# Optimization experiments

Hardware: AMD Instinct MI355X
Metric: run time of the kernel (lower is better)

## Reference

```python
import jax, jax.numpy as jnp
import numpy as np
from jax import lax

B, C, H, W = 16, 384, 28, 28
HEADS = 8


def _ln(x, g, b):
    mu = jnp.mean(x, axis=-1, keepdims=True)
    var = jnp.var(x, axis=-1, keepdims=True)
    return (x - mu) * lax.rsqrt(var + 1e-5) * g + b


def setup_inputs() -> dict:
    key = jax.random.key(0)
    ks = jax.random.split(key, 8)
    s = 0.02
    return {
        "cls_token": jax.random.normal(ks[0], (B, 1, C), dtype=jnp.float32),
        "x": jax.random.normal(ks[1], (B, C, H, W), dtype=jnp.float32),
        "conv_w": jax.random.normal(ks[2], (C, 1, 3, 3), dtype=jnp.float32) * s,
        "conv_b": jnp.zeros((C,), jnp.float32),
        "ln1_g": jnp.ones((C,), jnp.float32),
        "ln1_b": jnp.zeros((C,), jnp.float32),
        "qkv_w": jax.random.normal(ks[3], (3 * C, C), dtype=jnp.float32) * s,
        "proj_w": jax.random.normal(ks[4], (C, C), dtype=jnp.float32) * s,
        "proj_b": jnp.zeros((C,), jnp.float32),
        "ln2_g": jnp.ones((C,), jnp.float32),
        "ln2_b": jnp.zeros((C,), jnp.float32),
        "fc1_w": jax.random.normal(ks[5], (4 * C, C), dtype=jnp.float32) * s,
        "fc1_b": jnp.zeros((4 * C,), jnp.float32),
        "fc2_w": jax.random.normal(ks[6], (C, 4 * C), dtype=jnp.float32) * s,
        "fc2_b": jnp.zeros((C,), jnp.float32),
    }


def reference(cls_token, x, conv_w, conv_b, ln1_g, ln1_b, qkv_w, proj_w, proj_b,
              ln2_g, ln2_b, fc1_w, fc1_b, fc2_w, fc2_b):
    Bv, Cv, Hv, Wv = x.shape
    h = HEADS
    d = Cv // h
    # depthwise 3x3 positional conv (groups=dim), residual add
    pe = lax.conv_general_dilated(
        x, conv_w, window_strides=(1, 1), padding="SAME",
        feature_group_count=Cv,
        dimension_numbers=("NCHW", "OIHW", "NCHW")) + conv_b[None, :, None, None]
    x = x + pe
    x_patch = x.reshape(Bv, Cv, Hv * Wv).transpose(0, 2, 1)  # [B, HW, C]
    xc = jnp.concatenate([cls_token, x_patch], axis=1)       # [B, N, C]
    N = xc.shape[1]

    # --- Attention with inline global_attn stats (first-call / int sentinel path) ---
    y = _ln(xc, ln1_g, ln1_b)
    qkv = (y @ qkv_w.T).reshape(Bv, N, 3, h, d)
    q = qkv[:, :, 0].transpose(0, 2, 1, 3)  # [B, h, N, d]
    k = qkv[:, :, 1].transpose(0, 2, 1, 3)
    v = qkv[:, :, 2].transpose(0, 2, 1, 3)
    scale = d ** -0.5
    attn = jax.nn.softmax(jnp.einsum("bhnd,bhmd->bhnm", q, k) * scale, axis=-1)
    # per-token global attention statistic: mean over heads of cls row (excl. cls)
    global_attn = jnp.mean(attn[:, :, 0, 1:], axis=1)  # [B, N-1]
    o = jnp.einsum("bhnm,bhmd->bhnd", attn, v).transpose(0, 2, 1, 3).reshape(Bv, N, Cv)
    xc = xc + (o @ proj_w.T + proj_b)

    # --- MLP (GELU exact, matching torch nn.GELU default) ---
    y2 = _ln(xc, ln2_g, ln2_b)
    m = jax.nn.gelu(y2 @ fc1_w.T + fc1_b, approximate=False) @ fc2_w.T + fc2_b
    xc = xc + m

    cls_out = xc[:, :1]                                            # [B, 1, C]
    x_out = xc[:, 1:].transpose(0, 2, 1).reshape(Bv, Cv, Hv, Wv)    # [B, C, H, W]
    return cls_out, x_out, global_attn
```

## Files before the change

### kernel.cpp

```cpp
#include <hip/hip_runtime.h>
#include <hip/hip_bf16.h>

#define DI __device__ __forceinline__

typedef __attribute__((ext_vector_type(4))) float f32x4;
typedef __attribute__((ext_vector_type(8))) short bf16x8;
typedef __attribute__((ext_vector_type(4))) short bf16x4;

static constexpr int CB = 16;
static constexpr int CC = 384;
static constexpr int CH = 28, CW = 28;
static constexpr int CD = 48;
static constexpr int CN = 785;
static constexpr int CM = CB * CN;
static constexpr int C3 = 3 * CC;
static constexpr int CF = 4 * CC;
static constexpr int HW = CH * CW;
static constexpr int NP = 832;

DI short f2b(float f) {
  __hip_bfloat16 h = __float2bfloat16(f);
  return *reinterpret_cast<short*>(&h);
}
DI float b2f(short s) {
  union { unsigned u; float f; } x;
  x.u = ((unsigned)(unsigned short)s) << 16;
  return x.f;
}

DI void gload16(const short* g, short* l) {
  __builtin_amdgcn_global_load_lds((const __attribute__((address_space(1))) void*)g,
                                   (__attribute__((address_space(3))) void*)l, 16, 0, 0);
}

__global__ void k_misc(const float* __restrict__ cls, float* __restrict__ xc,
                       float* __restrict__ ga) {
  const int gid = blockIdx.x * 256 + threadIdx.x;
  if (gid < CB * HW) ga[gid] = 0.f;
  if (gid < CB * CC) {
    const int b = gid / CC, c = gid % CC;
    xc[((size_t)b * CN) * CC + c] = cls[gid];
  }
}

__global__ void k_wconv(const float* __restrict__ s0, const float* __restrict__ s1,
                        const float* __restrict__ s2, const float* __restrict__ s3,
                        short* __restrict__ dst) {
  const int gid = (blockIdx.x * 256 + threadIdx.x) * 4;
  if (gid >= 1769472) return;
  const float* s; int off;
  if (gid < 442368)       { s = s0; off = gid; }
  else if (gid < 589824)  { s = s1; off = gid - 442368; }
  else if (gid < 1179648) { s = s2; off = gid - 589824; }
  else                    { s = s3; off = gid - 1179648; }
  f32x4 v = *(const f32x4*)(s + off);
  bf16x4 o;
#pragma unroll
  for (int i = 0; i < 4; i++) o[i] = f2b(v[i]);
  *(bf16x4*)(dst + gid) = o;
}

__global__ __launch_bounds__(256) void k_conv_t(const float* __restrict__ x,
                                                const float* __restrict__ cw,
                                                const float* __restrict__ cb,
                                                float* __restrict__ xc) {
  __shared__ float T[64][65];
  __shared__ float Wc[64 * 9];
  __shared__ float Cbs[64];
  const int b = blockIdx.z;
  const int cc = blockIdx.y * 64;
  const int hw0 = blockIdx.x * 64;
  const int t = threadIdx.x;
  const int hwi = t & 63, ci0 = t >> 6;
  const int hw = hw0 + hwi;
  const int yy = hw / CW, xx = hw % CW;
  const int ci2 = t & 63, hb2 = t >> 6;

  for (int i = t; i < 64 * 9; i += 256) Wc[i] = cw[cc * 9 + i];
  if (t < 64) Cbs[t] = cb[cc + t];
  __syncthreads();
  if (hw < HW) {
#pragma unroll
    for (int j = 0; j < 16; j++) {
      const int cl = ci0 * 16 + j;
      const float* xp = x + ((size_t)(b * CC + cc + cl)) * HW;
      float acc = Cbs[cl];
      const float center = xp[yy * CW + xx];
#pragma unroll
      for (int ky = 0; ky < 3; ky++) {
        const int iy = yy + ky - 1;
        if (iy < 0 || iy >= CH) continue;
#pragma unroll
        for (int kx = 0; kx < 3; kx++) {
          const int ix = xx + kx - 1;
          if (ix < 0 || ix >= CW) continue;
          acc += Wc[cl * 9 + ky * 3 + kx] * xp[iy * CW + ix];
        }
      }
      T[cl][hwi] = center + acc;
    }
  }
  __syncthreads();
#pragma unroll
  for (int j = 0; j < 16; j++) {
    const int hwl = hb2 + j * 4;
    if (hw0 + hwl < HW)
      xc[((size_t)b * CN + 1 + hw0 + hwl) * CC + cc + ci2] = T[ci2][hwl];
  }
}

__global__ __launch_bounds__(256) void k_ln(const float* __restrict__ xin,
                                            const float* __restrict__ g,
                                            const float* __restrict__ bta,
                                            short* __restrict__ y, int Mtot) {
  const int row = blockIdx.x * 4 + (threadIdx.x >> 6);
  const int l = threadIdx.x & 63;
  if (row >= Mtot) return;
  const float* xr = xin + (size_t)row * CC;
  float v[6], s = 0.f, ss = 0.f;
#pragma unroll
  for (int i = 0; i < 6; i++) {
    v[i] = xr[l + i * 64];
    s += v[i];
    ss += v[i] * v[i];
  }
#pragma unroll
  for (int m = 1; m < 64; m <<= 1) { s += __shfl_xor(s, m); ss += __shfl_xor(ss, m); }
  const float mu = s * (1.f / CC);
  const float var = ss * (1.f / CC) - mu * mu;
  const float r = rsqrtf(var + 1e-5f);
#pragma unroll
  for (int i = 0; i < 6; i++) {
    const int c = l + i * 64;
    y[(size_t)row * CC + c] = f2b((v[i] - mu) * r * g[c] + bta[c]);
  }
}

template <int DOGELU, int DORES, int DOBIAS, int OUTBF>
__global__ __launch_bounds__(256) void k_gemm(const short* __restrict__ A,
                                              const short* __restrict__ W,
                                              const float* __restrict__ bias,
                                              const float* __restrict__ resid,
                                              void* __restrict__ out_,
                                              int M, int N, int K) {
  __shared__ short As[128 * 32];
  __shared__ short Bs[128 * 32];
  const int bm = blockIdx.x * 128, bn = blockIdx.y * 128;
  const int t = threadIdx.x, w = t >> 6, l = t & 63, g = l >> 4, li = l & 15;
  const int wm = (w >> 1) * 64, wn = (w & 1) * 64;

  const int srow = l >> 2;
  const int scol = (l & 3) * 8;
  const short* aSrc[2]; const short* bSrc[2];
  short* aDst[2]; short* bDst[2];
#pragma unroll
  for (int j = 0; j < 2; j++) {
    int arow = bm + w * 32 + j * 16 + srow; if (arow > M - 1) arow = M - 1;
    aSrc[j] = A + (size_t)arow * K + scol;
    aDst[j] = &As[(w * 32 + j * 16) * 32];
    const int brow = bn + w * 32 + j * 16 + srow;
    bSrc[j] = W + (size_t)brow * K + scol;
    bDst[j] = &Bs[(w * 32 + j * 16) * 32];
  }

  f32x4 acc[4][4] = {};
  const int nkt = K / 32;
  for (int kt = 0; kt < nkt; kt++) {
#pragma unroll
    for (int j = 0; j < 2; j++) {
      gload16(aSrc[j], aDst[j]);
      gload16(bSrc[j], bDst[j]);
      aSrc[j] += 32; bSrc[j] += 32;
    }
    __syncthreads();
    bf16x8 af[4], bf[4];
#pragma unroll
    for (int mi = 0; mi < 4; mi++)
      af[mi] = *(const bf16x8*)&As[(wm + mi * 16 + li) * 32 + g * 8];
#pragma unroll
    for (int ni = 0; ni < 4; ni++)
      bf[ni] = *(const bf16x8*)&Bs[(wn + ni * 16 + li) * 32 + g * 8];
#pragma unroll
    for (int mi = 0; mi < 4; mi++)
#pragma unroll
      for (int ni = 0; ni < 4; ni++)
        acc[mi][ni] = __builtin_amdgcn_mfma_f32_16x16x32_bf16(af[mi], bf[ni], acc[mi][ni], 0, 0, 0);
    __syncthreads();
  }

#pragma unroll
  for (int mi = 0; mi < 4; mi++)
#pragma unroll
    for (int ni = 0; ni < 4; ni++) {
      const int col = bn + wn + ni * 16 + li;
      float bv = 0.f;
      if constexpr (DOBIAS) bv = bias[col];
#pragma unroll
      for (int r = 0; r < 4; r++) {
        const int row = bm + wm + mi * 16 + g * 4 + r;
        if (row < M) {
          float v = acc[mi][ni][r] + bv;
          if constexpr (DOGELU) v = 0.5f * v * (1.f + erff(v * 0.7071067811865475f));
          if constexpr (DORES) v += resid[(size_t)row * N + col];
          if constexpr (OUTBF)
            ((short*)out_)[(size_t)row * N + col] = f2b(v);
          else
            ((float*)out_)[(size_t)row * N + col] = v;
        }
      }
    }
}

__global__ __launch_bounds__(256) void k_vt(const short* __restrict__ qkv,
                                            short* __restrict__ vt) {
  __shared__ short Tl[48 * 71];
  const int n0 = blockIdx.x * 64;
  const int bh = blockIdx.y;
  const int b = bh >> 3, h = bh & 7;
  const int t = threadIdx.x;
  const size_t bbase = (size_t)b * CN;
#pragma unroll
  for (int it = 0; it < 2; it++) {
    const int gi = t + it * 256;
    if (gi < 384) {
      const int nrel = gi / 6, dg = gi % 6;
      const int n = n0 + nrel;
      bf16x8 val = {};
      if (n < CN)
        val = *(const bf16x8*)(qkv + (bbase + n) * C3 + 2 * CC + h * CD + dg * 8);
#pragma unroll
      for (int i = 0; i < 8; i++) Tl[(dg * 8 + i) * 71 + nrel] = val[i];
    }
  }
  __syncthreads();
#pragma unroll
  for (int it = 0; it < 2; it++) {
    const int gj = t + it * 256;
    if (gj < 384) {
      const int d = gj >> 3, ng = gj & 7;
      bf16x8 v;
#pragma unroll
      for (int i = 0; i < 8; i++) v[i] = Tl[d * 71 + ng * 8 + i];
      *(bf16x8*)(vt + ((size_t)bh * CD + d) * NP + n0 + ng * 8) = v;
    }
  }
}

__global__ __launch_bounds__(256) void k_attn(const short* __restrict__ qkv,
                                              const short* __restrict__ vt,
                                              short* __restrict__ o) {
  __shared__ short Ks[64 * 48];
  __shared__ short Vs[48 * 64];
  const int f = blockIdx.x;
  const int xslot = f & 7, grp = f >> 3;
  const int bh = xslot + 8 * (grp & 15);
  const int qt = grp >> 4;
  const int b = bh >> 3, h = bh & 7;
  const int q0 = qt * 64;
  const int t = threadIdx.x, w = t >> 6, l = t & 63, g = l >> 4, li = l & 15;
  const size_t bbase = (size_t)b * CN;

  const int qrow = q0 + w * 16 + li;
  const int qr = qrow > CN - 1 ? CN - 1 : qrow;
  const short* qb = qkv + (bbase + qr) * C3 + h * CD;
  bf16x8 qf0 = *(const bf16x8*)(qb + g * 8);
  bf16x8 qf1 = {};
  if (g < 2) qf1 = *(const bf16x8*)(qb + 32 + g * 8);

  float mr = -1e30f, ls = 0.f;
  f32x4 oa[3] = {};
  const float scale = 0.14433756729740643f;

  const int krow0 = t / 6, kcg0 = t % 6;
  const int krow1 = (t + 256) / 6, kcg1 = (t + 256) % 6;
  const int vd0 = t >> 3, vkvg0 = t & 7;
  const int vd1 = (t + 256) >> 3, vkvg1 = (t + 256) & 7;
  const short* kbase = qkv + bbase * C3 + CC + h * CD;
  const short* vbase = vt + (size_t)bh * CD * NP;

  bf16x8 kr0 = {}, kr1 = {}, vr0 = {}, vr1 = {};
  kr0 = *(const bf16x8*)(kbase + (size_t)min(krow0, CN - 1) * C3 + kcg0 * 8);
  vr0 = *(const bf16x8*)(vbase + vd0 * NP + vkvg0 * 8);
  if (t < 128) {
    kr1 = *(const bf16x8*)(kbase + (size_t)min(krow1, CN - 1) * C3 + kcg1 * 8);
    vr1 = *(const bf16x8*)(vbase + vd1 * NP + vkvg1 * 8);
  }

  for (int kt = 0; kt < 13; kt++) {
    const int kv0 = kt * 64;
    __syncthreads();
    *(bf16x8*)((char*)Ks + ((krow0 * 96 + kcg0 * 16) ^ ((krow0 & 7) << 4))) = kr0;
    *(bf16x8*)((char*)Vs + ((vd0 * 128 + vkvg0 * 16) ^ ((vd0 & 7) << 4))) = vr0;
    if (t < 128) {
      *(bf16x8*)((char*)Ks + ((krow1 * 96 + kcg1 * 16) ^ ((krow1 & 7) << 4))) = kr1;
      *(bf16x8*)((char*)Vs + ((vd1 * 128 + vkvg1 * 16) ^ ((vd1 & 7) << 4))) = vr1;
    }
    __syncthreads();
    if (kt < 12) {
      const int kn = kv0 + 64;
      kr0 = *(const bf16x8*)(kbase + (size_t)min(kn + krow0, CN - 1) * C3 + kcg0 * 8);
      vr0 = *(const bf16x8*)(vbase + vd0 * NP + kn + vkvg0 * 8);
      if (t < 128) {
        kr1 = *(const bf16x8*)(kbase + (size_t)min(kn + krow1, CN - 1) * C3 + kcg1 * 8);
        vr1 = *(const bf16x8*)(vbase + vd1 * NP + kn + vkvg1 * 8);
      }
    }

    f32x4 s[4];
    __builtin_amdgcn_s_setprio(1);
#pragma unroll
    for (int ni = 0; ni < 4; ni++) {
      const int krw = ni * 16 + li;
      const int sw = (krw & 7) << 4;
      bf16x8 kf0 = *(const bf16x8*)((char*)Ks + ((krw * 96 + g * 16) ^ sw));
      bf16x8 kf1 = {};
      if (g < 2) kf1 = *(const bf16x8*)((char*)Ks + ((krw * 96 + 64 + g * 16) ^ sw));
      f32x4 acc = {};
      acc = __builtin_amdgcn_mfma_f32_16x16x32_bf16(kf0, qf0, acc, 0, 0, 0);
      acc = __builtin_amdgcn_mfma_f32_16x16x32_bf16(kf1, qf1, acc, 0, 0, 0);
      s[ni] = acc;
    }
    __builtin_amdgcn_s_setprio(0);

    float mt = -1e30f;
#pragma unroll
    for (int ni = 0; ni < 4; ni++)
#pragma unroll
      for (int r = 0; r < 4; r++) {
        const int kva = kv0 + ni * 16 + g * 4 + r;
        const float v = (kva < CN) ? s[ni][r] * scale : -1e30f;
        s[ni][r] = v;
        mt = fmaxf(mt, v);
      }
    mt = fmaxf(mt, __shfl_xor(mt, 16));
    mt = fmaxf(mt, __shfl_xor(mt, 32));
    const float mn = fmaxf(mr, mt);
    const float al = __expf(mr - mn);
    mr = mn;
    float ps = 0.f;
#pragma unroll
    for (int ni = 0; ni < 4; ni++)
#pragma unroll
      for (int r = 0; r < 4; r++) {
        const float p = __expf(s[ni][r] - mn);
        s[ni][r] = p;
        ps += p;
      }
    ps += __shfl_xor(ps, 16);
    ps += __shfl_xor(ps, 32);
    ls = ls * al + ps;

    const int sb = (l & 48) + ((l & 48) >> 2);
    float ar[4];
#pragma unroll
    for (int r = 0; r < 4; r++) ar[r] = __shfl(al, sb + r);
#pragma unroll
    for (int d = 0; d < 3; d++)
#pragma unroll
      for (int r = 0; r < 4; r++) oa[d][r] *= ar[r];

    bf16x8 pa[2];
#pragma unroll
    for (int ks = 0; ks < 2; ks++)
#pragma unroll
      for (int i = 0; i < 8; i++)
        pa[ks][i] = f2b(i < 4 ? s[2 * ks][i] : s[2 * ks + 1][i - 4]);

    __builtin_amdgcn_s_setprio(1);
#pragma unroll
    for (int d = 0; d < 3; d++) {
      const int drow = d * 16 + li;
      const int sw = (drow & 7) << 4;
#pragma unroll
      for (int ks = 0; ks < 2; ks++) {
        bf16x4 lo = *(const bf16x4*)((char*)Vs + ((drow * 128 + ks * 64 + g * 8) ^ sw));
        bf16x4 hi = *(const bf16x4*)((char*)Vs + ((drow * 128 + ks * 64 + 32 + g * 8) ^ sw));
        bf16x8 vb;
#pragma unroll
        for (int i = 0; i < 4; i++) { vb[i] = lo[i]; vb[4 + i] = hi[i]; }
        oa[d] = __builtin_amdgcn_mfma_f32_16x16x32_bf16(pa[ks], vb, oa[d], 0, 0, 0);
      }
    }
    __builtin_amdgcn_s_setprio(0);
  }

  const int sb = (l & 48) + ((l & 48) >> 2);
  float lr[4];
#pragma unroll
  for (int r = 0; r < 4; r++) lr[r] = __shfl(ls, sb + r);
#pragma unroll
  for (int d = 0; d < 3; d++)
#pragma unroll
    for (int r = 0; r < 4; r++) {
      const int n = q0 + w * 16 + g * 4 + r;
      if (n < CN)
        o[(bbase + n) * CC + h * CD + d * 16 + li] = f2b(oa[d][r] / lr[r]);
    }
}

__global__ __launch_bounds__(256) void k_gattn(const short* __restrict__ qkv,
                                               float* __restrict__ ga) {
  const int b = blockIdx.x >> 3, h = blockIdx.x & 7;
  __shared__ float red[4];
  const int t = threadIdx.x;
  const size_t bbase = (size_t)b * CN;
  const short* q0 = qkv + bbase * C3 + h * CD;
  float qv[CD];
#pragma unroll
  for (int i = 0; i < CD; i++) qv[i] = b2f(q0[i]);
  float lg[4], ev[4];
  float lmax = -1e30f;
#pragma unroll
  for (int j = 0; j < 4; j++) {
    const int m = t + j * 256;
    if (m < CN) {
      const short* kr = qkv + (bbase + m) * C3 + CC + h * CD;
      float acc = 0.f;
#pragma unroll
      for (int i = 0; i < CD; i++) acc += qv[i] * b2f(kr[i]);
      lg[j] = acc * 0.14433756729740643f;
      lmax = fmaxf(lmax, lg[j]);
    } else lg[j] = -1e30f;
  }
  for (int msk = 1; msk < 64; msk <<= 1) lmax = fmaxf(lmax, __shfl_xor(lmax, msk));
  if ((t & 63) == 0) red[t >> 6] = lmax;
  __syncthreads();
  lmax = fmaxf(fmaxf(red[0], red[1]), fmaxf(red[2], red[3]));
  __syncthreads();
  float es = 0.f;
#pragma unroll
  for (int j = 0; j < 4; j++) {
    ev[j] = (t + j * 256 < CN) ? __expf(lg[j] - lmax) : 0.f;
    es += ev[j];
  }
  for (int msk = 1; msk < 64; msk <<= 1) es += __shfl_xor(es, msk);
  if ((t & 63) == 0) red[t >> 6] = es;
  __syncthreads();
  es = red[0] + red[1] + red[2] + red[3];
  const float inv = 0.125f / es;
#pragma unroll
  for (int j = 0; j < 4; j++) {
    const int m = t + j * 256;
    if (m >= 1 && m < CN) atomicAdd(&ga[b * HW + m - 1], ev[j] * inv);
  }
}

__global__ __launch_bounds__(256) void k_out(const float* __restrict__ xc,
                                             float* __restrict__ outp) {
  const int b = blockIdx.y, tile = blockIdx.x, t = threadIdx.x;
  if (tile == 78) {
    for (int i = t; i < CC; i += 256)
      outp[b * CC + i] = xc[((size_t)b * CN) * CC + i];
    return;
  }
  __shared__ float T[64][65];
  const int ct = tile / 13, ht = tile % 13;
  const int c0 = ct * 64, hw0 = ht * 64;
  const int ci = t & 63, hb = t >> 6;
  for (int j = 0; j < 16; j++) {
    const int hwl = hb + j * 4;
    if (hw0 + hwl < HW)
      T[ci][hwl] = xc[((size_t)b * CN + 1 + hw0 + hwl) * CC + c0 + ci];
  }
  __syncthreads();
  const int hi = t & 63, cb2 = t >> 6;
  float* xo = outp + CB * CC;
  for (int j = 0; j < 16; j++) {
    const int cl = cb2 + j * 4;
    if (hw0 + hi < HW)
      xo[((size_t)(b * CC + c0 + cl)) * HW + hw0 + hi] = T[cl][hi];
  }
}

extern "C" void kernel_launch(void* const* d_in, const int* in_sizes, int n_in,
                              void* d_out, int out_size, void* d_ws, size_t ws_size,
                              hipStream_t stream) {
  const float* cls    = (const float*)d_in[0];
  const float* x      = (const float*)d_in[1];
  const float* conv_w = (const float*)d_in[2];
  const float* conv_b = (const float*)d_in[3];
  const float* ln1_g  = (const float*)d_in[4];
  const float* ln1_b  = (const float*)d_in[5];
  const float* qkv_w  = (const float*)d_in[6];
  const float* proj_w = (const float*)d_in[7];
  const float* proj_b = (const float*)d_in[8];
  const float* ln2_g  = (const float*)d_in[9];
  const float* ln2_b  = (const float*)d_in[10];
  const float* fc1_w  = (const float*)d_in[11];
  const float* fc1_b  = (const float*)d_in[12];
  const float* fc2_w  = (const float*)d_in[13];
  const float* fc2_b  = (const float*)d_in[14];

  float* outf = (float*)d_out;
  float* ga = outf + (size_t)CB * CC + (size_t)CB * CC * HW;
  short* vtb = (short*)(outf + CB * CC);

  char* ws = (char*)d_ws;
  float* xc   = (float*)ws;
  short* y    = (short*)(ws + 19292160ULL);
  short* qkvb = (short*)(ws + 28938240ULL);
  short* o    = (short*)(ws + 57876480ULL);
  short* m1   = (short*)(ws + 28938240ULL);
  short* wbuf = (short*)(ws + 67522560ULL);
  short* qkv_wb = wbuf;
  short* proj_wb = wbuf + 442368;
  short* fc1_wb  = wbuf + 589824;
  short* fc2_wb  = wbuf + 1179648;

  const int thr = 256;
  k_misc<<<49, thr, 0, stream>>>(cls, xc, ga);
  k_wconv<<<1728, thr, 0, stream>>>(qkv_w, proj_w, fc1_w, fc2_w, wbuf);
  k_conv_t<<<dim3(13, 6, CB), thr, 0, stream>>>(x, conv_w, conv_b, xc);
  k_ln<<<CM / 4, thr, 0, stream>>>(xc, ln1_g, ln1_b, y, CM);
  k_gemm<0, 0, 0, 1><<<dim3(99, C3 / 128), thr, 0, stream>>>(
      y, qkv_wb, nullptr, nullptr, qkvb, CM, C3, CC);
  k_vt<<<dim3(13, CB * 8), thr, 0, stream>>>(qkvb, vtb);
  k_attn<<<1664, thr, 0, stream>>>(qkvb, vtb, o);
  k_gattn<<<CB * 8, thr, 0, stream>>>(qkvb, ga);
  k_gemm<0, 1, 1, 0><<<dim3(99, CC / 128), thr, 0, stream>>>(
      o, proj_wb, proj_b, xc, xc, CM, CC, CC);
  k_ln<<<CM / 4, thr, 0, stream>>>(xc, ln2_g, ln2_b, y, CM);
  k_gemm<1, 0, 1, 1><<<dim3(99, CF / 128), thr, 0, stream>>>(
      y, fc1_wb, fc1_b, nullptr, m1, CM, CF, CC);
  k_gemm<0, 1, 1, 0><<<dim3(99, CC / 128), thr, 0, stream>>>(
      m1, fc2_wb, fc2_b, xc, xc, CM, CC, CF);
  k_out<<<dim3(79, CB), thr, 0, stream>>>(xc, outf);
}
```

Baseline: 398.0 us.

## Double-buffer GEMM shared tiles and use 64-row tiles for narrow GEMMs

The GEMM kernel now keeps two shared-memory buffers and issues the global-to-LDS loads for the next K tile before the current tile's MFMAs run, replacing the load/sync/compute/sync serialization. The row tile size becomes a template parameter. The proj and fc2 GEMMs, which have only 384 output columns, switch to 64-row tiles so they launch twice as many blocks and fill more CUs. The cost is double the LDS per block and fewer MFMAs per block for the narrow GEMMs.

```diff
diff --git a/kernel.cpp b/kernel.cpp
--- a/kernel.cpp
+++ b/kernel.cpp
@@ -136,60 +136,75 @@
   }
 }
 
-template <int DOGELU, int DORES, int DOBIAS, int OUTBF>
+template <int BM, int DOGELU, int DORES, int DOBIAS, int OUTBF>
 __global__ __launch_bounds__(256) void k_gemm(const short* __restrict__ A,
                                               const short* __restrict__ W,
                                               const float* __restrict__ bias,
                                               const float* __restrict__ resid,
                                               void* __restrict__ out_,
                                               int M, int N, int K) {
-  __shared__ short As[128 * 32];
-  __shared__ short Bs[128 * 32];
-  const int bm = blockIdx.x * 128, bn = blockIdx.y * 128;
+  constexpr int MI = BM / 32;
+  constexpr int ACALLS = BM / 64;
+  __shared__ short As[2 * BM * 32];
+  __shared__ short Bs[2 * 128 * 32];
+  const int bm = blockIdx.x * BM, bn = blockIdx.y * 128;
   const int t = threadIdx.x, w = t >> 6, l = t & 63, g = l >> 4, li = l & 15;
-  const int wm = (w >> 1) * 64, wn = (w & 1) * 64;
+  const int wm = (w >> 1) * (BM / 2), wn = (w & 1) * 64;
 
   const int srow = l >> 2;
   const int scol = (l & 3) * 8;
-  const short* aSrc[2]; const short* bSrc[2];
-  short* aDst[2]; short* bDst[2];
+  const short* aSrc[ACALLS]; int aOff[ACALLS];
+#pragma unroll
+  for (int j = 0; j < ACALLS; j++) {
+    int arow = bm + w * (BM / 4) + j * 16 + srow; if (arow > M - 1) arow = M - 1;
+    aSrc[j] = A + (size_t)arow * K + scol;
+    aOff[j] = (w * (BM / 4) + j * 16) * 32;
+  }
+  const short* bSrc[2]; int bOff[2];
 #pragma unroll
   for (int j = 0; j < 2; j++) {
-    int arow = bm + w * 32 + j * 16 + srow; if (arow > M - 1) arow = M - 1;
-    aSrc[j] = A + (size_t)arow * K + scol;
-    aDst[j] = &As[(w * 32 + j * 16) * 32];
     const int brow = bn + w * 32 + j * 16 + srow;
     bSrc[j] = W + (size_t)brow * K + scol;
-    bDst[j] = &Bs[(w * 32 + j * 16) * 32];
-  }
-
-  f32x4 acc[4][4] = {};
+    bOff[j] = (w * 32 + j * 16) * 32;
+  }
+
+  auto stage = [&](int buf, int kt) {
+    const int ko = kt * 32;
+#pragma unroll
+    for (int j = 0; j < ACALLS; j++)
+      gload16(aSrc[j] + ko, &As[buf * (BM * 32)] + aOff[j]);
+#pragma unroll
+    for (int j = 0; j < 2; j++)
+      gload16(bSrc[j] + ko, &Bs[buf * (128 * 32)] + bOff[j]);
+  };
+
+  f32x4 acc[MI][4] = {};
   const int nkt = K / 32;
+  stage(0, 0);
+  __syncthreads();
+  int cur = 0;
   for (int kt = 0; kt < nkt; kt++) {
-#pragma unroll
-    for (int j = 0; j < 2; j++) {
-      gload16(aSrc[j], aDst[j]);
-      gload16(bSrc[j], bDst[j]);
-      aSrc[j] += 32; bSrc[j] += 32;
-    }
-    __syncthreads();
-    bf16x8 af[4], bf[4];
-#pragma unroll
-    for (int mi = 0; mi < 4; mi++)
-      af[mi] = *(const bf16x8*)&As[(wm + mi * 16 + li) * 32 + g * 8];
+    if (kt + 1 < nkt) stage(cur ^ 1, kt + 1);
+    const short* Ab = &As[cur * (BM * 32)];
+    const short* Bb = &Bs[cur * (128 * 32)];
+    bf16x8 af[MI], bf[4];
+#pragma unroll
+    for (int mi = 0; mi < MI; mi++)
+      af[mi] = *(const bf16x8*)&Ab[(wm + mi * 16 + li) * 32 + g * 8];
 #pragma unroll
     for (int ni = 0; ni < 4; ni++)
-      bf[ni] = *(const bf16x8*)&Bs[(wn + ni * 16 + li) * 32 + g * 8];
-#pragma unroll
-    for (int mi = 0; mi < 4; mi++)
+      bf[ni] = *(const bf16x8*)&Bb[(wn + ni * 16 + li) * 32 + g * 8];
+#pragma unroll
+    for (int mi = 0; mi < MI; mi++)
 #pragma unroll
       for (int ni = 0; ni < 4; ni++)
         acc[mi][ni] = __builtin_amdgcn_mfma_f32_16x16x32_bf16(af[mi], bf[ni], acc[mi][ni], 0, 0, 0);
     __syncthreads();
-  }
-
-#pragma unroll
-  for (int mi = 0; mi < 4; mi++)
+    cur ^= 1;
+  }
+
+#pragma unroll
+  for (int mi = 0; mi < MI; mi++)
 #pragma unroll
     for (int ni = 0; ni < 4; ni++) {
       const int col = bn + wn + ni * 16 + li;
@@ -512,17 +527,17 @@
   k_wconv<<<1728, thr, 0, stream>>>(qkv_w, proj_w, fc1_w, fc2_w, wbuf);
   k_conv_t<<<dim3(13, 6, CB), thr, 0, stream>>>(x, conv_w, conv_b, xc);
   k_ln<<<CM / 4, thr, 0, stream>>>(xc, ln1_g, ln1_b, y, CM);
-  k_gemm<0, 0, 0, 1><<<dim3(99, C3 / 128), thr, 0, stream>>>(
+  k_gemm<128, 0, 0, 0, 1><<<dim3(99, C3 / 128), thr, 0, stream>>>(
       y, qkv_wb, nullptr, nullptr, qkvb, CM, C3, CC);
   k_vt<<<dim3(13, CB * 8), thr, 0, stream>>>(qkvb, vtb);
   k_attn<<<1664, thr, 0, stream>>>(qkvb, vtb, o);
   k_gattn<<<CB * 8, thr, 0, stream>>>(qkvb, ga);
-  k_gemm<0, 1, 1, 0><<<dim3(99, CC / 128), thr, 0, stream>>>(
+  k_gemm<64, 0, 1, 1, 0><<<dim3(197, CC / 128), thr, 0, stream>>>(
       o, proj_wb, proj_b, xc, xc, CM, CC, CC);
   k_ln<<<CM / 4, thr, 0, stream>>>(xc, ln2_g, ln2_b, y, CM);
-  k_gemm<1, 0, 1, 1><<<dim3(99, CF / 128), thr, 0, stream>>>(
+  k_gemm<128, 1, 0, 1, 1><<<dim3(99, CF / 128), thr, 0, stream>>>(
       y, fc1_wb, fc1_b, nullptr, m1, CM, CF, CC);
-  k_gemm<0, 1, 1, 0><<<dim3(99, CC / 128), thr, 0, stream>>>(
+  k_gemm<64, 0, 1, 1, 0><<<dim3(197, CC / 128), thr, 0, stream>>>(
       m1, fc2_wb, fc2_b, xc, xc, CM, CC, CF);
   k_out<<<dim3(79, CB), thr, 0, stream>>>(xc, outf);
 }
```

New measurement: 370.2 us. 7.0% less time.
